# Kernel optimization log

Hardware: AMD Instinct MI355X
Metric: run time of the kernel (lower is better)

The kernel has to match this reference:

```python
import jax, jax.numpy as jnp
import numpy as np

BN_EPS = 1e-5


def _bn(h, gamma, beta):
    # BatchNorm1d training mode on [N, C]: biased batch stats per channel
    mu = h.mean(axis=0)
    var = h.var(axis=0)  # ddof=0 (biased), matching torch forward
    return (h - mu) * jax.lax.rsqrt(var + BN_EPS) * gamma + beta


def setup_inputs() -> dict:
    key = jax.random.key(0)
    ks = jax.random.split(key, 4)
    N_parent, C_in, C_out = 65536, 128, 64
    N_child = 8 * N_parent
    x = jax.random.normal(ks[0], (N_parent, C_in), dtype=jnp.float32)
    # octree neighbor table for the 3^3=27-tap conv at depth+1
    neigh = jax.random.randint(ks[1], (N_child, 27), 0, N_child, dtype=jnp.int32)
    W_up = jax.random.normal(ks[2], (8, C_in, C_out), dtype=jnp.float32) * 0.05
    W_conv = jax.random.normal(ks[3], (27, C_out, C_out), dtype=jnp.float32) * 0.05
    gamma1 = jnp.ones((C_out,), jnp.float32)
    beta1 = jnp.zeros((C_out,), jnp.float32)
    gamma2 = jnp.ones((C_out,), jnp.float32)
    beta2 = jnp.zeros((C_out,), jnp.float32)
    return {"x": x, "neigh": neigh, "W_up": W_up, "W_conv": W_conv,
            "gamma1": gamma1, "beta1": beta1, "gamma2": gamma2, "beta2": beta2}


def reference(x, neigh, W_up, W_conv, gamma1, beta1, gamma2, beta2):
    C_out = W_up.shape[-1]
    # OctreeDeconv k=2 s=2: each parent p emits 8 children, child c = 8p + octant,
    # out[c] = x[p] @ W_up[octant]
    y = jnp.einsum('pc,kcd->pkd', x, W_up).reshape(-1, C_out)  # [N_child, C_out]
    y = jax.nn.elu(_bn(y, gamma1, beta1))
    # OctreeConv k=3: 27-tap gather-matmul-accumulate (fixed small tap loop;
    # avoids materializing the [N_child, 27, C] gathered tensor)
    acc = jnp.zeros_like(y)
    for k in range(27):
        acc = acc + y[neigh[:, k]] @ W_conv[k]
    out = jax.nn.elu(_bn(acc, gamma2, beta2))
    return out
```

## Files before the change

### kernel.cpp

```cpp
#include <hip/hip_runtime.h>


#define N_PARENT 65536
#define C_IN     128
#define C_OUT    64
#define N_CHILD  (N_PARENT * 8)
#define TAPS     27
#define NBINS    64

typedef __bf16 bf16x8 __attribute__((ext_vector_type(8)));
typedef float  f32x4  __attribute__((ext_vector_type(4)));
typedef int    i32x4  __attribute__((ext_vector_type(4)));

#define Y_OFF     0u
#define WTUP_OFF  67108864u
#define W8CV_OFF  67239936u
#define CHMAX_OFF 67350528u
#define CHMIN_OFF 67350784u
#define SINV_OFF  67351040u
#define SCL_OFF   67351296u
#define S1_OFF    67351552u
#define S2_OFF    67384320u
#define AB1_OFF   67417088u
#define AB2_OFF   67417600u
#define ZERO_LEN  (67418112u - CHMAX_OFF)

__device__ __forceinline__ float elu_f(float f) {
    return f > 0.f ? f : (__expf(f) - 1.f);
}
__device__ __forceinline__ unsigned fkey(float f) {
    unsigned b = __float_as_uint(f);
    return (b & 0x80000000u) ? ~b : (b | 0x80000000u);
}
__device__ __forceinline__ float fdec(unsigned k) {
    unsigned b = (k & 0x80000000u) ? (k & 0x7fffffffu) : ~k;
    return __uint_as_float(b);
}

__global__ __launch_bounds__(256) void prep_wup(const float* __restrict__ wup,
                                                __bf16* __restrict__ wtup) {
    int i = blockIdx.x * 256 + threadIdx.x;
    int o = i >> 13, rem = i & 8191, n = rem >> 7, k = rem & 127;
    wtup[i] = (__bf16)wup[o * 8192 + k * 64 + n];
}

__global__ __launch_bounds__(256) void deconv_bn_stats(
    const float* __restrict__ x, const __bf16* __restrict__ wtup,
    __bf16* __restrict__ y, float* __restrict__ bins,
    unsigned* __restrict__ chmax, unsigned* __restrict__ chmin) {
    __shared__ float ssum[64], ssq[64];
    __shared__ unsigned smax[64], smin[64];
    int tid = threadIdx.x;
    int wave = tid >> 6, lane = tid & 63, lr = lane & 15, lg = lane >> 4;
    int p0 = blockIdx.x * 16;

    if (tid < 64) { ssum[tid] = 0.f; ssq[tid] = 0.f; smax[tid] = 0u; smin[tid] = 0xFFFFFFFFu; }

    const float* xrow = x + (size_t)(p0 + lr) * C_IN;
    bf16x8 afr[4];
#pragma unroll
    for (int ks = 0; ks < 4; ++ks) {
        const float* src = xrow + ks * 32 + lg * 8;
        f32x4 u0 = *(const f32x4*)(src);
        f32x4 u1 = *(const f32x4*)(src + 4);
        bf16x8 a;
#pragma unroll
        for (int i = 0; i < 4; ++i) { a[i] = (__bf16)u0[i]; a[4 + i] = (__bf16)u1[i]; }
        afr[ks] = a;
    }

    float lsum[4] = {0.f, 0.f, 0.f, 0.f}, lsq[4] = {0.f, 0.f, 0.f, 0.f};
    float hx[4] = {-3e38f, -3e38f, -3e38f, -3e38f};
    float hn[4] = {3e38f, 3e38f, 3e38f, 3e38f};
#pragma unroll
    for (int oo = 0; oo < 2; ++oo) {
        int oct = wave * 2 + oo;
#pragma unroll
        for (int nt = 0; nt < 4; ++nt) {
            f32x4 acc = {0.f, 0.f, 0.f, 0.f};
#pragma unroll
            for (int ks = 0; ks < 4; ++ks) {
                const __bf16* bp = wtup + ((size_t)(oct * 64 + nt * 16 + lr) * C_IN + ks * 32 + lg * 8);
                bf16x8 b = *(const bf16x8*)bp;
                acc = __builtin_amdgcn_mfma_f32_16x16x32_bf16(afr[ks], b, acc, 0, 0, 0);
            }
#pragma unroll
            for (int r = 0; r < 4; ++r) {
                int parent = p0 + lg * 4 + r;
                int child = parent * 8 + oct;
                float v = acc[r];
                y[(size_t)child * 64 + nt * 16 + lr] = (__bf16)v;
                lsum[nt] += v; lsq[nt] += v * v;
                hx[nt] = fmaxf(hx[nt], v); hn[nt] = fminf(hn[nt], v);
            }
        }
    }
    __syncthreads();
#pragma unroll
    for (int nt = 0; nt < 4; ++nt) {
        atomicAdd(&ssum[nt * 16 + lr], lsum[nt]);
        atomicAdd(&ssq[nt * 16 + lr], lsq[nt]);
        atomicMax(&smax[nt * 16 + lr], fkey(hx[nt]));
        atomicMin(&smin[nt * 16 + lr], fkey(hn[nt]));
    }
    __syncthreads();
    if (tid < 64) {
        float* b = bins + (size_t)(blockIdx.x & (NBINS - 1)) * 128;
        atomicAdd(&b[tid], ssum[tid]);
        atomicAdd(&b[64 + tid], ssq[tid]);
        atomicMax(&chmax[tid], smax[tid]);
        atomicMin(&chmin[tid], smin[tid]);
    }
}

__global__ void finalize_bn1(const float* __restrict__ bins,
                             const float* __restrict__ gamma,
                             const float* __restrict__ beta,
                             const unsigned* __restrict__ chmax,
                             const unsigned* __restrict__ chmin,
                             float* __restrict__ ab,
                             float* __restrict__ sinv, float* __restrict__ scl,
                             float invN) {
    int c = threadIdx.x;
    float s = 0.f, q = 0.f;
    for (int b = 0; b < NBINS; ++b) { s += bins[b * 128 + c]; q += bins[b * 128 + 64 + c]; }
    float mu = s * invN;
    float var = q * invN - mu * mu;
    float rstd = rsqrtf(var + 1e-5f);
    float a = gamma[c] * rstd;
    float b = beta[c] - mu * a;
    ab[c] = a;
    ab[64 + c] = b;
    float hmx = fdec(chmax[c]), hmn = fdec(chmin[c]);
    float t0 = a * hmx + b, t1 = a * hmn + b;
    float fhi = elu_f(fmaxf(t0, t1));
    float flo = elu_f(fminf(t0, t1));
    float chabs = fmaxf(fmaxf(fhi, -flo), 1e-6f) * 1.005f;
    sinv[c] = 127.f / chabs;
    scl[c] = chabs * (1.f / 127.f);
}

__global__ void finalize_stats(const float* __restrict__ bins,
                               const float* __restrict__ gamma,
                               const float* __restrict__ beta,
                               float* __restrict__ ab, float invN) {
    int c = threadIdx.x;
    float s = 0.f, q = 0.f;
    for (int b = 0; b < NBINS; ++b) { s += bins[b * 128 + c]; q += bins[b * 128 + 64 + c]; }
    float mu = s * invN;
    float var = q * invN - mu * mu;
    float rstd = rsqrtf(var + 1e-5f);
    float a = gamma[c] * rstd;
    ab[c] = a;
    ab[64 + c] = beta[c] - mu * a;
}

__global__ __launch_bounds__(256) void prep_w8(const float* __restrict__ wcv,
                                               const float* __restrict__ scl,
                                               signed char* __restrict__ w8) {
    __shared__ float scl_s[64];
    __shared__ float red[4];
    __shared__ float tds;
    int d = blockIdx.x, t = threadIdx.x;
    if (t < 64) scl_s[t] = scl[t];
    __syncthreads();
    float m = 0.f;
    for (int i = t; i < 1728; i += 256) m = fmaxf(m, fabsf(wcv[i * 64 + d]) * scl_s[i & 63]);
#pragma unroll
    for (int dd = 1; dd < 64; dd <<= 1) m = fmaxf(m, __shfl_xor(m, dd));
    if ((t & 63) == 0) red[t >> 6] = m;
    __syncthreads();
    if (t == 0) {
        float mm = fmaxf(fmaxf(red[0], red[1]), fmaxf(red[2], red[3]));
        tds = 127.f / fmaxf(mm, 1e-20f);
    }
    __syncthreads();
    float T = tds;
    for (int i = t; i < 1728; i += 256) {
        int k = i >> 6, c = i & 63;
        float v = wcv[i * 64 + d] * scl_s[c] * T;
        w8[k * 4096 + d * 64 + c] = (signed char)(int)rintf(v);
    }
}

__global__ __launch_bounds__(256) void bn_elu_quant(char* __restrict__ ybuf,
                                                    const float* __restrict__ ab,
                                                    const float* __restrict__ sinv) {
    int gt = blockIdx.x * 256 + threadIdx.x;
    int row = gt >> 2, q = gt & 3;
    int c0 = q * 16;
    const __bf16* yr = (const __bf16*)(ybuf + (size_t)row * 128) + c0;
    bf16x8 h0 = *(const bf16x8*)(yr);
    bf16x8 h1 = *(const bf16x8*)(yr + 8);
    float v[16];
#pragma unroll
    for (int j = 0; j < 8; ++j) {
        float f = (float)h0[j] * ab[c0 + j] + ab[64 + c0 + j];
        v[j] = elu_f(f) * sinv[c0 + j];
    }
#pragma unroll
    for (int j = 0; j < 8; ++j) {
        float f = (float)h1[j] * ab[c0 + 8 + j] + ab[64 + c0 + 8 + j];
        v[8 + j] = elu_f(f) * sinv[c0 + 8 + j];
    }
    i32x4 pk;
#pragma unroll
    for (int w = 0; w < 4; ++w) {
        int acc = 0;
#pragma unroll
        for (int j = 0; j < 4; ++j) {
            float vc = fminf(fmaxf(v[w * 4 + j], -127.f), 127.f);
            int qv = (int)rintf(vc);
            acc |= (qv & 255) << (8 * j);
        }
        pk[w] = acc;
    }
    *(i32x4*)(ybuf + (size_t)row * 128 + q * 16) = pk;
}

__global__ __launch_bounds__(256, 4) void conv_bn_stats(
    const char* __restrict__ ybuf, const int* __restrict__ neigh,
    const signed char* __restrict__ w8,
    float* __restrict__ out, float* __restrict__ bins) {
    __shared__ __align__(16) int idxb_s[4][32 * TAPS];
    __shared__ float ssum[64], ssq[64];
    int tid = threadIdx.x;
    int wave = tid >> 6, lane = tid & 63, lr = lane & 15, lg = lane >> 4;
    int wr0 = blockIdx.x * 128 + wave * 32;

    if (tid < 64) { ssum[tid] = 0.f; ssq[tid] = 0.f; }

    int* idxb = idxb_s[wave];

    {
        int base_w = wr0 * TAPS;
#pragma unroll
        for (int j = 0; j < 14; ++j) {
            int w = j * 64 + lane;
            if (w < 32 * TAPS) idxb[w] = neigh[base_w + w];
        }
    }
    asm volatile("s_waitcnt vmcnt(0) lgkmcnt(0)" ::: "memory");
    __builtin_amdgcn_sched_barrier(0);

    i32x4 iacc[2][4];
#pragma unroll
    for (int mt = 0; mt < 2; ++mt)
#pragma unroll
        for (int nt = 0; nt < 4; ++nt) iacc[mt][nt] = (i32x4){0, 0, 0, 0};

    const signed char* w8l = w8 + lr * 64 + lg * 16;

    i32x4 abuf[2][2];
    i32x4 bbuf[2][4];
    int icur[2];

    {
        int i00 = idxb[lr * TAPS + 0], i01 = idxb[(16 + lr) * TAPS + 0];
        abuf[0][0] = *(const i32x4*)(ybuf + (size_t)(unsigned)i00 * 128 + lg * 16);
        abuf[0][1] = *(const i32x4*)(ybuf + (size_t)(unsigned)i01 * 128 + lg * 16);
#pragma unroll
        for (int nt = 0; nt < 4; ++nt) bbuf[0][nt] = *(const i32x4*)(w8l + nt * 1024);
        __builtin_amdgcn_sched_barrier(0);
        int i10 = idxb[lr * TAPS + 1], i11 = idxb[(16 + lr) * TAPS + 1];
        abuf[1][0] = *(const i32x4*)(ybuf + (size_t)(unsigned)i10 * 128 + lg * 16);
        abuf[1][1] = *(const i32x4*)(ybuf + (size_t)(unsigned)i11 * 128 + lg * 16);
#pragma unroll
        for (int nt = 0; nt < 4; ++nt) bbuf[1][nt] = *(const i32x4*)(w8l + 4096 + nt * 1024);
        __builtin_amdgcn_sched_barrier(0);
        icur[0] = idxb[lr * TAPS + 2];
        icur[1] = idxb[(16 + lr) * TAPS + 2];
    }

#pragma unroll
    for (int k = 0; k < TAPS; ++k) {
        const int p = k & 1;
        if (k < TAPS - 1) { asm volatile("s_waitcnt vmcnt(6)" ::: "memory"); }
        else              { asm volatile("s_waitcnt vmcnt(0)" ::: "memory"); }
        __builtin_amdgcn_sched_barrier(0);
#pragma unroll
        for (int nt = 0; nt < 4; ++nt) {
            iacc[0][nt] = __builtin_amdgcn_mfma_i32_16x16x64_i8(abuf[p][0], bbuf[p][nt], iacc[0][nt], 0, 0, 0);
            iacc[1][nt] = __builtin_amdgcn_mfma_i32_16x16x64_i8(abuf[p][1], bbuf[p][nt], iacc[1][nt], 0, 0, 0);
        }
        if (k + 2 < TAPS) {
            abuf[p][0] = *(const i32x4*)(ybuf + (size_t)(unsigned)icur[0] * 128 + lg * 16);
            abuf[p][1] = *(const i32x4*)(ybuf + (size_t)(unsigned)icur[1] * 128 + lg * 16);
#pragma unroll
            for (int nt = 0; nt < 4; ++nt)
                bbuf[p][nt] = *(const i32x4*)(w8l + (k + 2) * 4096 + nt * 1024);
            if (k + 3 < TAPS) {
                icur[0] = idxb[lr * TAPS + (k + 3)];
                icur[1] = idxb[(16 + lr) * TAPS + (k + 3)];
            }
        }
    }

    float lsum[4] = {0.f, 0.f, 0.f, 0.f}, lsq[4] = {0.f, 0.f, 0.f, 0.f};
#pragma unroll
    for (int mt = 0; mt < 2; ++mt)
#pragma unroll
        for (int nt = 0; nt < 4; ++nt)
#pragma unroll
            for (int r = 0; r < 4; ++r) {
                float v = (float)iacc[mt][nt][r];
                int row = wr0 + mt * 16 + lg * 4 + r;
                out[(size_t)row * C_OUT + nt * 16 + lr] = v;
                lsum[nt] += v; lsq[nt] += v * v;
            }
    __syncthreads();
#pragma unroll
    for (int nt = 0; nt < 4; ++nt) {
        atomicAdd(&ssum[nt * 16 + lr], lsum[nt]);
        atomicAdd(&ssq[nt * 16 + lr], lsq[nt]);
    }
    __syncthreads();
    if (tid < 64) {
        float* b = bins + (size_t)(blockIdx.x & (NBINS - 1)) * 128;
        atomicAdd(&b[tid], ssum[tid]);
        atomicAdd(&b[64 + tid], ssq[tid]);
    }
}

__global__ __launch_bounds__(256) void bn_elu_out(float* __restrict__ out,
                                                  const float* __restrict__ ab) {
    int tid = blockIdx.x * 256 + threadIdx.x;
    int c0 = (tid * 4) & 63;
    float av[4], bv[4];
#pragma unroll
    for (int j = 0; j < 4; ++j) { av[j] = ab[c0 + j]; bv[j] = ab[64 + c0 + j]; }
#pragma unroll
    for (int t = 0; t < 8; ++t) {
        size_t e = ((size_t)t * 1048576 + tid) * 4;
        f32x4 v = *(const f32x4*)(out + e);
        f32x4 o;
#pragma unroll
        for (int j = 0; j < 4; ++j) o[j] = elu_f(v[j] * av[j] + bv[j]);
        *(f32x4*)(out + e) = o;
    }
}

extern "C" void kernel_launch(void* const* d_in, const int* in_sizes, int n_in,
                              void* d_out, int out_size, void* d_ws, size_t ws_size,
                              hipStream_t stream) {
    const float* x     = (const float*)d_in[0];
    const int*   neigh = (const int*)d_in[1];
    const float* wup   = (const float*)d_in[2];
    const float* wcv   = (const float*)d_in[3];
    const float* g1    = (const float*)d_in[4];
    const float* b1    = (const float*)d_in[5];
    const float* g2    = (const float*)d_in[6];
    const float* b2    = (const float*)d_in[7];
    float* out = (float*)d_out;

    char* ws = (char*)d_ws;
    char*        ybuf  = ws + Y_OFF;
    __bf16*      wtup  = (__bf16*)(ws + WTUP_OFF);
    signed char* w8    = (signed char*)(ws + W8CV_OFF);
    unsigned*    chmax = (unsigned*)(ws + CHMAX_OFF);
    unsigned*    chmin = (unsigned*)(ws + CHMIN_OFF);
    float*       sinv  = (float*)(ws + SINV_OFF);
    float*       scl   = (float*)(ws + SCL_OFF);
    float*       bins1 = (float*)(ws + S1_OFF);
    float*       bins2 = (float*)(ws + S2_OFF);
    float*       ab1   = (float*)(ws + AB1_OFF);
    float*       ab2   = (float*)(ws + AB2_OFF);

    hipMemsetAsync(ws + CHMAX_OFF, 0, ZERO_LEN, stream);
    hipMemsetAsync(ws + CHMIN_OFF, 0xFF, 256, stream);

    prep_wup<<<256, 256, 0, stream>>>(wup, wtup);
    deconv_bn_stats<<<N_PARENT / 16, 256, 0, stream>>>(x, wtup, (__bf16*)ybuf, bins1, chmax, chmin);
    finalize_bn1<<<1, 64, 0, stream>>>(bins1, g1, b1, chmax, chmin, ab1, sinv, scl, 1.f / (float)N_CHILD);
    prep_w8<<<64, 256, 0, stream>>>(wcv, scl, w8);
    bn_elu_quant<<<8192, 256, 0, stream>>>(ybuf, ab1, sinv);
    conv_bn_stats<<<N_CHILD / 128, 256, 0, stream>>>(ybuf, neigh, w8, out, bins2);
    finalize_stats<<<1, 64, 0, stream>>>(bins2, g2, b2, ab2, 1.f / (float)N_CHILD);
    bn_elu_out<<<4096, 256, 0, stream>>>(out, ab2);
}
```

Before: 465.8 us.

## Recompute deconv in quant pass instead of storing bf16 intermediate; pack int8 rows densely

The first deconv pass now only gathers BN statistics and no longer writes the bf16 intermediate. A new kernel recomputes the deconv MFMA, applies BN1+ELU, quantizes to int8 and writes a compact 64-byte-per-row buffer through an LDS transpose. The conv gather stride drops from 128 to 64 bytes. This removes a 64MB write and read of y at the cost of redoing the small deconv matmul. The quantization headroom factor is also tightened.

Result: slower. 497.8 us (+6.9%).

```diff
diff --git a/kernel.cpp b/kernel.cpp
--- a/kernel.cpp
+++ b/kernel.cpp
@@ -11,19 +11,20 @@
 typedef __bf16 bf16x8 __attribute__((ext_vector_type(8)));
 typedef float  f32x4  __attribute__((ext_vector_type(4)));
 typedef int    i32x4  __attribute__((ext_vector_type(4)));
-
-#define Y_OFF     0u
-#define WTUP_OFF  67108864u
-#define W8CV_OFF  67239936u
-#define CHMAX_OFF 67350528u
-#define CHMIN_OFF 67350784u
-#define SINV_OFF  67351040u
-#define SCL_OFF   67351296u
-#define S1_OFF    67351552u
-#define S2_OFF    67384320u
-#define AB1_OFF   67417088u
-#define AB2_OFF   67417600u
-#define ZERO_LEN  (67418112u - CHMAX_OFF)
+typedef unsigned u32x4 __attribute__((ext_vector_type(4)));
+
+#define Y8_OFF    0u
+#define WTUP_OFF  33554432u
+#define W8CV_OFF  33685504u
+#define CHMAX_OFF 33796096u
+#define CHMIN_OFF 33796352u
+#define SINV_OFF  33796608u
+#define SCL_OFF   33796864u
+#define S1_OFF    33797120u
+#define S2_OFF    33829888u
+#define AB1_OFF   33862656u
+#define AB2_OFF   33863168u
+#define ZERO_LEN  (33863680u - CHMAX_OFF)
 
 __device__ __forceinline__ float elu_f(float f) {
     return f > 0.f ? f : (__expf(f) - 1.f);
@@ -44,9 +45,9 @@
     wtup[i] = (__bf16)wup[o * 8192 + k * 64 + n];
 }
 
-__global__ __launch_bounds__(256) void deconv_bn_stats(
+__global__ __launch_bounds__(256) void deconv_stats(
     const float* __restrict__ x, const __bf16* __restrict__ wtup,
-    __bf16* __restrict__ y, float* __restrict__ bins,
+    float* __restrict__ bins,
     unsigned* __restrict__ chmax, unsigned* __restrict__ chmin) {
     __shared__ float ssum[64], ssq[64];
     __shared__ unsigned smax[64], smin[64];
@@ -86,10 +87,7 @@
             }
 #pragma unroll
             for (int r = 0; r < 4; ++r) {
-                int parent = p0 + lg * 4 + r;
-                int child = parent * 8 + oct;
                 float v = acc[r];
-                y[(size_t)child * 64 + nt * 16 + lr] = (__bf16)v;
                 lsum[nt] += v; lsq[nt] += v * v;
                 hx[nt] = fmaxf(hx[nt], v); hn[nt] = fminf(hn[nt], v);
             }
@@ -135,7 +133,7 @@
     float t0 = a * hmx + b, t1 = a * hmn + b;
     float fhi = elu_f(fmaxf(t0, t1));
     float flo = elu_f(fminf(t0, t1));
-    float chabs = fmaxf(fmaxf(fhi, -flo), 1e-6f) * 1.005f;
+    float chabs = fmaxf(fmaxf(fhi, -flo), 1e-6f) * 1.0005f;
     sinv[c] = 127.f / chabs;
     scl[c] = chabs * (1.f / 127.f);
 }
@@ -183,39 +181,67 @@
     }
 }
 
-__global__ __launch_bounds__(256) void bn_elu_quant(char* __restrict__ ybuf,
-                                                    const float* __restrict__ ab,
-                                                    const float* __restrict__ sinv) {
-    int gt = blockIdx.x * 256 + threadIdx.x;
-    int row = gt >> 2, q = gt & 3;
-    int c0 = q * 16;
-    const __bf16* yr = (const __bf16*)(ybuf + (size_t)row * 128) + c0;
-    bf16x8 h0 = *(const bf16x8*)(yr);
-    bf16x8 h1 = *(const bf16x8*)(yr + 8);
-    float v[16];
-#pragma unroll
-    for (int j = 0; j < 8; ++j) {
-        float f = (float)h0[j] * ab[c0 + j] + ab[64 + c0 + j];
-        v[j] = elu_f(f) * sinv[c0 + j];
-    }
-#pragma unroll
-    for (int j = 0; j < 8; ++j) {
-        float f = (float)h1[j] * ab[c0 + 8 + j] + ab[64 + c0 + 8 + j];
-        v[8 + j] = elu_f(f) * sinv[c0 + 8 + j];
-    }
-    i32x4 pk;
-#pragma unroll
-    for (int w = 0; w < 4; ++w) {
-        int acc = 0;
-#pragma unroll
-        for (int j = 0; j < 4; ++j) {
-            float vc = fminf(fmaxf(v[w * 4 + j], -127.f), 127.f);
-            int qv = (int)rintf(vc);
-            acc |= (qv & 255) << (8 * j);
+__global__ __launch_bounds__(256) void quant_recompute(
+    const float* __restrict__ x, const __bf16* __restrict__ wtup,
+    const float* __restrict__ ab, const float* __restrict__ sinv,
+    signed char* __restrict__ y8) {
+    __shared__ unsigned ytile[128][17];
+    int tid = threadIdx.x;
+    int wave = tid >> 6, lane = tid & 63, lr = lane & 15, lg = lane >> 4;
+    int p0 = blockIdx.x * 16;
+
+    const float* xrow = x + (size_t)(p0 + lr) * C_IN;
+    bf16x8 xf[4];
+#pragma unroll
+    for (int ks = 0; ks < 4; ++ks) {
+        const float* src = xrow + ks * 32 + lg * 8;
+        f32x4 u0 = *(const f32x4*)(src);
+        f32x4 u1 = *(const f32x4*)(src + 4);
+        bf16x8 a;
+#pragma unroll
+        for (int i = 0; i < 4; ++i) { a[i] = (__bf16)u0[i]; a[4 + i] = (__bf16)u1[i]; }
+        xf[ks] = a;
+    }
+
+#pragma unroll
+    for (int oo = 0; oo < 2; ++oo) {
+        int oct = wave * 2 + oo;
+#pragma unroll
+        for (int nt = 0; nt < 4; ++nt) {
+            f32x4 acc = {0.f, 0.f, 0.f, 0.f};
+#pragma unroll
+            for (int ks = 0; ks < 4; ++ks) {
+                const __bf16* wp = wtup + ((size_t)(oct * 64 + nt * 16 + lr) * C_IN + ks * 32 + lg * 8);
+                bf16x8 wf = *(const bf16x8*)wp;
+                acc = __builtin_amdgcn_mfma_f32_16x16x32_bf16(wf, xf[ks], acc, 0, 0, 0);
+            }
+            int n0 = nt * 16 + lg * 4;
+            f32x4 a4 = *(const f32x4*)(ab + n0);
+            f32x4 b4 = *(const f32x4*)(ab + 64 + n0);
+            f32x4 s4 = *(const f32x4*)(sinv + n0);
+            unsigned pack = 0;
+#pragma unroll
+            for (int r = 0; r < 4; ++r) {
+                float f = acc[r] * a4[r] + b4[r];
+                float v = elu_f(f) * s4[r];
+                v = fminf(fmaxf(v, -127.f), 127.f);
+                int qv = (int)rintf(v);
+                pack |= (unsigned)(qv & 255) << (8 * r);
+            }
+            ytile[lr * 8 + oct][nt * 4 + lg] = pack;
         }
-        pk[w] = acc;
-    }
-    *(i32x4*)(ybuf + (size_t)row * 128 + q * 16) = pk;
+    }
+    __syncthreads();
+    int cl = tid >> 1, half = tid & 1;
+    unsigned w[8];
+#pragma unroll
+    for (int j = 0; j < 8; ++j) w[j] = ytile[cl][half * 8 + j];
+    u32x4 v0, v1;
+#pragma unroll
+    for (int j = 0; j < 4; ++j) { v0[j] = w[j]; v1[j] = w[4 + j]; }
+    char* dst = (char*)y8 + ((size_t)(p0 * 8 + cl) * 64 + half * 32);
+    *(u32x4*)dst = v0;
+    *(u32x4*)(dst + 16) = v1;
 }
 
 __global__ __launch_bounds__(256, 4) void conv_bn_stats(
@@ -257,14 +283,14 @@
 
     {
         int i00 = idxb[lr * TAPS + 0], i01 = idxb[(16 + lr) * TAPS + 0];
-        abuf[0][0] = *(const i32x4*)(ybuf + (size_t)(unsigned)i00 * 128 + lg * 16);
-        abuf[0][1] = *(const i32x4*)(ybuf + (size_t)(unsigned)i01 * 128 + lg * 16);
+        abuf[0][0] = *(const i32x4*)(ybuf + (size_t)(unsigned)i00 * 64 + lg * 16);
+        abuf[0][1] = *(const i32x4*)(ybuf + (size_t)(unsigned)i01 * 64 + lg * 16);
 #pragma unroll
         for (int nt = 0; nt < 4; ++nt) bbuf[0][nt] = *(const i32x4*)(w8l + nt * 1024);
         __builtin_amdgcn_sched_barrier(0);
         int i10 = idxb[lr * TAPS + 1], i11 = idxb[(16 + lr) * TAPS + 1];
-        abuf[1][0] = *(const i32x4*)(ybuf + (size_t)(unsigned)i10 * 128 + lg * 16);
-        abuf[1][1] = *(const i32x4*)(ybuf + (size_t)(unsigned)i11 * 128 + lg * 16);
+        abuf[1][0] = *(const i32x4*)(ybuf + (size_t)(unsigned)i10 * 64 + lg * 16);
+        abuf[1][1] = *(const i32x4*)(ybuf + (size_t)(unsigned)i11 * 64 + lg * 16);
 #pragma unroll
         for (int nt = 0; nt < 4; ++nt) bbuf[1][nt] = *(const i32x4*)(w8l + 4096 + nt * 1024);
         __builtin_amdgcn_sched_barrier(0);
@@ -284,8 +310,8 @@
             iacc[1][nt] = __builtin_amdgcn_mfma_i32_16x16x64_i8(abuf[p][1], bbuf[p][nt], iacc[1][nt], 0, 0, 0);
         }
         if (k + 2 < TAPS) {
-            abuf[p][0] = *(const i32x4*)(ybuf + (size_t)(unsigned)icur[0] * 128 + lg * 16);
-            abuf[p][1] = *(const i32x4*)(ybuf + (size_t)(unsigned)icur[1] * 128 + lg * 16);
+            abuf[p][0] = *(const i32x4*)(ybuf + (size_t)(unsigned)icur[0] * 64 + lg * 16);
+            abuf[p][1] = *(const i32x4*)(ybuf + (size_t)(unsigned)icur[1] * 64 + lg * 16);
 #pragma unroll
             for (int nt = 0; nt < 4; ++nt)
                 bbuf[p][nt] = *(const i32x4*)(w8l + (k + 2) * 4096 + nt * 1024);
@@ -354,7 +380,7 @@
     float* out = (float*)d_out;
 
     char* ws = (char*)d_ws;
-    char*        ybuf  = ws + Y_OFF;
+    signed char* y8    = (signed char*)(ws + Y8_OFF);
     __bf16*      wtup  = (__bf16*)(ws + WTUP_OFF);
     signed char* w8    = (signed char*)(ws + W8CV_OFF);
     unsigned*    chmax = (unsigned*)(ws + CHMAX_OFF);
@@ -370,11 +396,11 @@
     hipMemsetAsync(ws + CHMIN_OFF, 0xFF, 256, stream);
 
     prep_wup<<<256, 256, 0, stream>>>(wup, wtup);
-    deconv_bn_stats<<<N_PARENT / 16, 256, 0, stream>>>(x, wtup, (__bf16*)ybuf, bins1, chmax, chmin);
+    deconv_stats<<<N_PARENT / 16, 256, 0, stream>>>(x, wtup, bins1, chmax, chmin);
     finalize_bn1<<<1, 64, 0, stream>>>(bins1, g1, b1, chmax, chmin, ab1, sinv, scl, 1.f / (float)N_CHILD);
     prep_w8<<<64, 256, 0, stream>>>(wcv, scl, w8);
-    bn_elu_quant<<<8192, 256, 0, stream>>>(ybuf, ab1, sinv);
-    conv_bn_stats<<<N_CHILD / 128, 256, 0, stream>>>(ybuf, neigh, w8, out, bins2);
+    quant_recompute<<<N_PARENT / 16, 256, 0, stream>>>(x, wtup, ab1, sinv, y8);
+    conv_bn_stats<<<N_CHILD / 128, 256, 0, stream>>>((const char*)y8, neigh, w8, out, bins2);
     finalize_stats<<<1, 64, 0, stream>>>(bins2, g2, b2, ab2, 1.f / (float)N_CHILD);
     bn_elu_out<<<4096, 256, 0, stream>>>(out, ab2);
 }
```

## Store deconv output as packed MFMA fragments and repack via LDS in quant

Applied to the files above, without the earlier changes.

The deconv kernel now writes each MFMA accumulator as a contiguous 8-byte packed bf16 fragment per lane, replacing scattered 2-byte stores at strided child rows. The quantization kernel reads these fragment blocks coalesced, applies BN+ELU+int8 quantization, transposes through shared memory, and writes int8 rows in a per-block layout. The conv kernel's gather uses a matching address function. This targets uncoalesced store traffic in the deconv, at the cost of an LDS transpose and more index arithmetic.

Measured after the change: 434.7 us. 6.7% less time.

```diff
diff --git a/kernel.cpp b/kernel.cpp
--- a/kernel.cpp
+++ b/kernel.cpp
@@ -11,8 +11,10 @@
 typedef __bf16 bf16x8 __attribute__((ext_vector_type(8)));
 typedef float  f32x4  __attribute__((ext_vector_type(4)));
 typedef int    i32x4  __attribute__((ext_vector_type(4)));
-
-#define Y_OFF     0u
+typedef unsigned u32x2 __attribute__((ext_vector_type(2)));
+typedef unsigned u32x4 __attribute__((ext_vector_type(4)));
+
+#define H_OFF     0u
 #define WTUP_OFF  67108864u
 #define W8CV_OFF  67239936u
 #define CHMAX_OFF 67350528u
@@ -36,6 +38,12 @@
     unsigned b = (k & 0x80000000u) ? (k & 0x7fffffffu) : ~k;
     return __uint_as_float(b);
 }
+__device__ __forceinline__ unsigned short bfb(float v) {
+    __bf16 b = (__bf16)v;
+    union { __bf16 b; unsigned short u; } c;
+    c.b = b;
+    return c.u;
+}
 
 __global__ __launch_bounds__(256) void prep_wup(const float* __restrict__ wup,
                                                 __bf16* __restrict__ wtup) {
@@ -46,7 +54,7 @@
 
 __global__ __launch_bounds__(256) void deconv_bn_stats(
     const float* __restrict__ x, const __bf16* __restrict__ wtup,
-    __bf16* __restrict__ y, float* __restrict__ bins,
+    char* __restrict__ hfrag, float* __restrict__ bins,
     unsigned* __restrict__ chmax, unsigned* __restrict__ chmin) {
     __shared__ float ssum[64], ssq[64];
     __shared__ unsigned smax[64], smin[64];
@@ -69,6 +77,7 @@
         afr[ks] = a;
     }
 
+    char* hblk = hfrag + (size_t)blockIdx.x * 16384;
     float lsum[4] = {0.f, 0.f, 0.f, 0.f}, lsq[4] = {0.f, 0.f, 0.f, 0.f};
     float hx[4] = {-3e38f, -3e38f, -3e38f, -3e38f};
     float hn[4] = {3e38f, 3e38f, 3e38f, 3e38f};
@@ -86,13 +95,14 @@
             }
 #pragma unroll
             for (int r = 0; r < 4; ++r) {
-                int parent = p0 + lg * 4 + r;
-                int child = parent * 8 + oct;
                 float v = acc[r];
-                y[(size_t)child * 64 + nt * 16 + lr] = (__bf16)v;
                 lsum[nt] += v; lsq[nt] += v * v;
                 hx[nt] = fmaxf(hx[nt], v); hn[nt] = fminf(hn[nt], v);
             }
+            u32x2 pk;
+            pk[0] = (unsigned)bfb(acc[0]) | ((unsigned)bfb(acc[1]) << 16);
+            pk[1] = (unsigned)bfb(acc[2]) | ((unsigned)bfb(acc[3]) << 16);
+            *(u32x2*)(hblk + ((oct * 4 + nt) * 64 + lane) * 8) = pk;
         }
     }
     __syncthreads();
@@ -183,39 +193,56 @@
     }
 }
 
-__global__ __launch_bounds__(256) void bn_elu_quant(char* __restrict__ ybuf,
-                                                    const float* __restrict__ ab,
-                                                    const float* __restrict__ sinv) {
-    int gt = blockIdx.x * 256 + threadIdx.x;
-    int row = gt >> 2, q = gt & 3;
-    int c0 = q * 16;
-    const __bf16* yr = (const __bf16*)(ybuf + (size_t)row * 128) + c0;
-    bf16x8 h0 = *(const bf16x8*)(yr);
-    bf16x8 h1 = *(const bf16x8*)(yr + 8);
-    float v[16];
-#pragma unroll
-    for (int j = 0; j < 8; ++j) {
-        float f = (float)h0[j] * ab[c0 + j] + ab[64 + c0 + j];
-        v[j] = elu_f(f) * sinv[c0 + j];
-    }
-#pragma unroll
-    for (int j = 0; j < 8; ++j) {
-        float f = (float)h1[j] * ab[c0 + 8 + j] + ab[64 + c0 + 8 + j];
-        v[8 + j] = elu_f(f) * sinv[c0 + 8 + j];
-    }
-    i32x4 pk;
-#pragma unroll
-    for (int w = 0; w < 4; ++w) {
-        int acc = 0;
-#pragma unroll
-        for (int j = 0; j < 4; ++j) {
-            float vc = fminf(fmaxf(v[w * 4 + j], -127.f), 127.f);
-            int qv = (int)rintf(vc);
-            acc |= (qv & 255) << (8 * j);
+__global__ __launch_bounds__(256) void quant_pack(char* __restrict__ hbuf,
+                                                  const float* __restrict__ ab,
+                                                  const float* __restrict__ sinv) {
+    __shared__ char y8t[128][68];
+    __shared__ float a_s[64], b_s[64], s_s[64];
+    int tid = threadIdx.x;
+    if (tid < 64) { a_s[tid] = ab[tid]; b_s[tid] = ab[64 + tid]; s_s[tid] = sinv[tid]; }
+    __syncthreads();
+
+    char* reg = hbuf + (size_t)blockIdx.x * 16384;
+#pragma unroll
+    for (int j = 0; j < 4; ++j) {
+        u32x4 v = *(const u32x4*)(reg + j * 4096 + tid * 16);
+        int u0 = j * 512 + tid * 2;
+#pragma unroll
+        for (int half = 0; half < 2; ++half) {
+            int u = u0 + half;
+            unsigned w0 = v[half * 2], w1 = v[half * 2 + 1];
+            int w8i = u >> 8, nt = (u >> 6) & 3, ln = u & 63;
+            int lr = ln & 15, lg = ln >> 4;
+            int col = nt * 16 + lr;
+            float a = a_s[col], b = b_s[col], s = s_s[col];
+            int cb = lg * 32 + w8i;
+            float fr[4];
+            fr[0] = __uint_as_float(w0 << 16);
+            fr[1] = __uint_as_float(w0 & 0xFFFF0000u);
+            fr[2] = __uint_as_float(w1 << 16);
+            fr[3] = __uint_as_float(w1 & 0xFFFF0000u);
+#pragma unroll
+            for (int r = 0; r < 4; ++r) {
+                float f = fr[r] * a + b;
+                float vq = elu_f(f) * s;
+                vq = fminf(fmaxf(vq, -127.f), 127.f);
+                int q = (int)rintf(vq);
+                y8t[cb + r * 8][col] = (char)q;
+            }
         }
-        pk[w] = acc;
-    }
-    *(i32x4*)(ybuf + (size_t)row * 128 + q * 16) = pk;
+    }
+    __syncthreads();
+    int cl = tid >> 1, half = tid & 1;
+    unsigned wv[8];
+#pragma unroll
+    for (int j = 0; j < 8; ++j)
+        wv[j] = *(const unsigned*)(&y8t[cl][half * 32 + j * 4]);
+    u32x4 v0, v1;
+#pragma unroll
+    for (int j = 0; j < 4; ++j) { v0[j] = wv[j]; v1[j] = wv[4 + j]; }
+    char* dst = reg + cl * 64 + half * 32;
+    *(u32x4*)dst = v0;
+    *(u32x4*)(dst + 16) = v1;
 }
 
 __global__ __launch_bounds__(256, 4) void conv_bn_stats(
@@ -243,6 +270,8 @@
     asm volatile("s_waitcnt vmcnt(0) lgkmcnt(0)" ::: "memory");
     __builtin_amdgcn_sched_barrier(0);
 
+#define YADDR(idx) (((size_t)((unsigned)(idx) >> 7) << 14) + (((unsigned)(idx) & 127u) << 6))
+
     i32x4 iacc[2][4];
 #pragma unroll
     for (int mt = 0; mt < 2; ++mt)
@@ -257,14 +286,14 @@
 
     {
         int i00 = idxb[lr * TAPS + 0], i01 = idxb[(16 + lr) * TAPS + 0];
-        abuf[0][0] = *(const i32x4*)(ybuf + (size_t)(unsigned)i00 * 128 + lg * 16);
-        abuf[0][1] = *(const i32x4*)(ybuf + (size_t)(unsigned)i01 * 128 + lg * 16);
+        abuf[0][0] = *(const i32x4*)(ybuf + YADDR(i00) + lg * 16);
+        abuf[0][1] = *(const i32x4*)(ybuf + YADDR(i01) + lg * 16);
 #pragma unroll
         for (int nt = 0; nt < 4; ++nt) bbuf[0][nt] = *(const i32x4*)(w8l + nt * 1024);
         __builtin_amdgcn_sched_barrier(0);
         int i10 = idxb[lr * TAPS + 1], i11 = idxb[(16 + lr) * TAPS + 1];
-        abuf[1][0] = *(const i32x4*)(ybuf + (size_t)(unsigned)i10 * 128 + lg * 16);
-        abuf[1][1] = *(const i32x4*)(ybuf + (size_t)(unsigned)i11 * 128 + lg * 16);
+        abuf[1][0] = *(const i32x4*)(ybuf + YADDR(i10) + lg * 16);
+        abuf[1][1] = *(const i32x4*)(ybuf + YADDR(i11) + lg * 16);
 #pragma unroll
         for (int nt = 0; nt < 4; ++nt) bbuf[1][nt] = *(const i32x4*)(w8l + 4096 + nt * 1024);
         __builtin_amdgcn_sched_barrier(0);
@@ -284,8 +313,8 @@
             iacc[1][nt] = __builtin_amdgcn_mfma_i32_16x16x64_i8(abuf[p][1], bbuf[p][nt], iacc[1][nt], 0, 0, 0);
         }
         if (k + 2 < TAPS) {
-            abuf[p][0] = *(const i32x4*)(ybuf + (size_t)(unsigned)icur[0] * 128 + lg * 16);
-            abuf[p][1] = *(const i32x4*)(ybuf + (size_t)(unsigned)icur[1] * 128 + lg * 16);
+            abuf[p][0] = *(const i32x4*)(ybuf + YADDR(icur[0]) + lg * 16);
+            abuf[p][1] = *(const i32x4*)(ybuf + YADDR(icur[1]) + lg * 16);
 #pragma unroll
             for (int nt = 0; nt < 4; ++nt)
                 bbuf[p][nt] = *(const i32x4*)(w8l + (k + 2) * 4096 + nt * 1024);
@@ -354,7 +383,7 @@
     float* out = (float*)d_out;
 
     char* ws = (char*)d_ws;
-    char*        ybuf  = ws + Y_OFF;
+    char*        hbuf  = ws + H_OFF;
     __bf16*      wtup  = (__bf16*)(ws + WTUP_OFF);
     signed char* w8    = (signed char*)(ws + W8CV_OFF);
     unsigned*    chmax = (unsigned*)(ws + CHMAX_OFF);
@@ -370,11 +399,11 @@
     hipMemsetAsync(ws + CHMIN_OFF, 0xFF, 256, stream);
 
     prep_wup<<<256, 256, 0, stream>>>(wup, wtup);
-    deconv_bn_stats<<<N_PARENT / 16, 256, 0, stream>>>(x, wtup, (__bf16*)ybuf, bins1, chmax, chmin);
+    deconv_bn_stats<<<N_PARENT / 16, 256, 0, stream>>>(x, wtup, hbuf, bins1, chmax, chmin);
     finalize_bn1<<<1, 64, 0, stream>>>(bins1, g1, b1, chmax, chmin, ab1, sinv, scl, 1.f / (float)N_CHILD);
     prep_w8<<<64, 256, 0, stream>>>(wcv, scl, w8);
-    bn_elu_quant<<<8192, 256, 0, stream>>>(ybuf, ab1, sinv);
-    conv_bn_stats<<<N_CHILD / 128, 256, 0, stream>>>(ybuf, neigh, w8, out, bins2);
+    quant_pack<<<N_PARENT / 16, 256, 0, stream>>>(hbuf, ab1, sinv);
+    conv_bn_stats<<<N_CHILD / 128, 256, 0, stream>>>((const char*)hbuf, neigh, w8, out, bins2);
     finalize_stats<<<1, 64, 0, stream>>>(bins2, g2, b2, ab2, 1.f / (float)N_CHILD);
     bn_elu_out<<<4096, 256, 0, stream>>>(out, ab2);
 }
```
